# Performance work log

Hardware: AMD Instinct MI355X
Metric: run time of the kernel (lower is better)

## Reference

```python
import jax, jax.numpy as jnp
import numpy as np

B, S, D, H = 2, 2048, 1024, 16
DK = D // H

def setup_inputs() -> dict:
    key = jax.random.key(0)
    ks = jax.random.split(key, 9)
    sc = 1.0 / np.sqrt(D)
    return {
        "query": jax.random.normal(ks[0], (B, S, D), jnp.float32),
        "key_": jax.random.normal(ks[1], (B, S, D), jnp.float32),
        "value": jax.random.normal(ks[2], (B, S, D), jnp.float32),
        "Wq": jax.random.normal(ks[3], (D, D), jnp.float32) * sc,
        "bq": jnp.zeros((D,), jnp.float32),
        "Wk": jax.random.normal(ks[4], (D, D), jnp.float32) * sc,
        "bk": jnp.zeros((D,), jnp.float32),
        "Wv": jax.random.normal(ks[5], (D, D), jnp.float32) * sc,
        "bv": jnp.zeros((D,), jnp.float32),
    }

def reference(query, key_, value, Wq, bq, Wk, bk, Wv, bv):
    # QKV projections -> [B, H, S, DK]
    def heads(x, W, b):
        return (x @ W + b).reshape(B, S, H, DK).transpose(0, 2, 1, 3)
    q = heads(query, Wq, bq)
    k = heads(key_, Wk, bk)
    v = heads(value, Wv, bv)
    scores = jnp.einsum('bhsd,bhtd->bhst', q, k) / jnp.sqrt(jnp.float32(DK))
    attn = jax.nn.softmax(scores, axis=-1)  # dropout = identity (eval)
    ctx = jnp.einsum('bhst,bhtd->bhsd', attn, v)
    return ctx.transpose(0, 2, 1, 3).reshape(B, S, D)
```

## Files before the change

### kernel.cpp

```cpp
#include <hip/hip_runtime.h>
#include <hip/hip_bf16.h>

typedef __bf16 bf16x4 __attribute__((ext_vector_type(4)));
typedef __bf16 bf16x8 __attribute__((ext_vector_type(8)));
typedef float  f32x4  __attribute__((ext_vector_type(4)));
typedef float  f32x16 __attribute__((ext_vector_type(16)));

constexpr int B = 2, S = 2048, D = 1024, H = 16, DK = 64;
constexpr int M = B * S;
constexpr int BH = B * H;

__device__ inline float fexp2(float x) {
#if __has_builtin(__builtin_amdgcn_exp2f)
  return __builtin_amdgcn_exp2f(x);
#else
  return exp2f(x);
#endif
}
__device__ inline float frcp(float x) {
#if __has_builtin(__builtin_amdgcn_rcpf)
  return __builtin_amdgcn_rcpf(x);
#else
  return 1.0f / x;
#endif
}
__device__ inline unsigned pk2(float lo, float hi) {
  union { __bf16 h[2]; unsigned u; } x;
  x.h[0] = (__bf16)lo; x.h[1] = (__bf16)hi;
  return x.u;
}

__global__ __launch_bounds__(256) void wtrans3(const float* __restrict__ w0,
                                               const float* __restrict__ w1,
                                               const float* __restrict__ w2,
                                               __bf16* __restrict__ t0,
                                               __bf16* __restrict__ t1,
                                               __bf16* __restrict__ t2) {
  int z = blockIdx.z;
  const float* W = z == 0 ? w0 : z == 1 ? w1 : w2;
  __bf16* WT = z == 0 ? t0 : z == 1 ? t1 : t2;
  __shared__ float t[32][33];
  int tx = threadIdx.x & 31, ty0 = threadIdx.x >> 5;
  int n0 = blockIdx.x * 32, k0 = blockIdx.y * 32;
#pragma unroll
  for (int i = 0; i < 4; ++i)
    t[ty0 + i * 8][tx] = W[(size_t)(k0 + ty0 + i * 8) * D + n0 + tx];
  __syncthreads();
#pragma unroll
  for (int i = 0; i < 4; ++i)
    WT[(size_t)(n0 + ty0 + i * 8) * D + k0 + tx] = (__bf16)t[tx][ty0 + i * 8];
}

constexpr int TM = 128, TN = 128, BK = 64;

__global__ __launch_bounds__(256, 3) void proj3(
    const float* __restrict__ X0, const float* __restrict__ X1,
    const float* __restrict__ X2, const __bf16* __restrict__ W0,
    const __bf16* __restrict__ W1, const __bf16* __restrict__ W2,
    const float* __restrict__ b0, const float* __restrict__ b1,
    const float* __restrict__ b2, __bf16* __restrict__ Qo,
    __bf16* __restrict__ Ko, __bf16* __restrict__ Vo) {
  __shared__ __align__(16) __bf16 As[TM * BK];
  __shared__ __align__(16) __bf16 Bs[2][TN * BK];
  int z = blockIdx.z;
  const float* A   = z == 0 ? X0 : z == 1 ? X1 : X2;
  const __bf16* BT = z == 0 ? W0 : z == 1 ? W1 : W2;
  const float* bias = z == 0 ? b0 : z == 1 ? b1 : b2;
  __bf16* out = z == 0 ? Qo : z == 1 ? Ko : Vo;
  int mode = (z == 2) ? 1 : 0;
  float osc = (z == 0) ? 0.18033688011112042f : 1.0f;

  int t = threadIdx.x;
  int fid = blockIdx.x;
  int xcd = fid & 7, slot = fid >> 3;
  int m0 = (xcd * 4 + (slot >> 3)) * TM;
  int n0 = (slot & 7) * TN;
  int w = t >> 6, lane = t & 63, c = lane & 15, g = lane >> 4;
  int wr = w >> 1, wc = w & 1;

  f32x4 acc[4][4];
#pragma unroll
  for (int i = 0; i < 4; ++i)
#pragma unroll
    for (int j = 0; j < 4; ++j) acc[i][j] = f32x4{0.f, 0.f, 0.f, 0.f};

  int srcoff = (((t & 7) ^ ((t >> 3) & 7)) << 4);
  int srow = t >> 3;
  const float* aptr[4];
  const __bf16* bptr[4];
#pragma unroll
  for (int i = 0; i < 4; ++i) {
    aptr[i] = A + (size_t)(m0 + i * 32 + srow) * D + (srcoff >> 1);
    bptr[i] = BT + (size_t)(n0 + i * 32 + srow) * D + (srcoff >> 1);
  }

  float4 pa[4][2];
#pragma unroll
  for (int i = 0; i < 4; ++i) {
    pa[i][0] = *(const float4*)(aptr[i]);
    pa[i][1] = *(const float4*)(aptr[i] + 4);
  }
#pragma unroll
  for (int i = 0; i < 4; ++i)
    __builtin_amdgcn_global_load_lds(
        (const __attribute__((address_space(1))) unsigned int*)(bptr[i]),
        (__attribute__((address_space(3))) unsigned int*)((char*)&Bs[0][0] + i * 4096 + t * 16), 16, 0, 0);

  int rswz = ((c & 7) << 4);

  int buf = 0;
  for (int kk = 0; kk < D; kk += BK, buf ^= 1) {
    if (kk + BK < D) {
#pragma unroll
      for (int i = 0; i < 4; ++i)
        __builtin_amdgcn_global_load_lds(
            (const __attribute__((address_space(1))) unsigned int*)(bptr[i] + kk + BK),
            (__attribute__((address_space(3))) unsigned int*)((char*)&Bs[buf ^ 1][0] + i * 4096 + t * 16), 16, 0, 0);
    }
#pragma unroll
    for (int i = 0; i < 4; ++i) {
      bf16x8 v;
      v[0] = (__bf16)pa[i][0].x; v[1] = (__bf16)pa[i][0].y;
      v[2] = (__bf16)pa[i][0].z; v[3] = (__bf16)pa[i][0].w;
      v[4] = (__bf16)pa[i][1].x; v[5] = (__bf16)pa[i][1].y;
      v[6] = (__bf16)pa[i][1].z; v[7] = (__bf16)pa[i][1].w;
      *(bf16x8*)((char*)As + i * 4096 + t * 16) = v;
    }
    if (kk + BK < D)
      asm volatile("s_waitcnt vmcnt(4) lgkmcnt(0)" ::: "memory");
    else
      asm volatile("s_waitcnt vmcnt(0) lgkmcnt(0)" ::: "memory");
    __builtin_amdgcn_s_barrier();
    __builtin_amdgcn_sched_barrier(0);

    if (kk + BK < D) {
#pragma unroll
      for (int i = 0; i < 4; ++i) {
        pa[i][0] = *(const float4*)(aptr[i] + kk + BK);
        pa[i][1] = *(const float4*)(aptr[i] + kk + BK + 4);
      }
    }

#pragma unroll
    for (int ks = 0; ks < 2; ++ks) {
      int cb = (ks * 64 + g * 16) ^ rswz;
      bf16x8 af[4], bf[4];
#pragma unroll
      for (int i = 0; i < 4; ++i)
        af[i] = *(const bf16x8*)((char*)As + (wr * 64 + i * 16 + c) * 128 + cb);
#pragma unroll
      for (int j = 0; j < 4; ++j)
        bf[j] = *(const bf16x8*)((char*)&Bs[buf][0] + (wc * 64 + j * 16 + c) * 128 + cb);
#pragma unroll
      for (int i = 0; i < 4; ++i)
#pragma unroll
        for (int j = 0; j < 4; ++j)
          acc[i][j] = __builtin_amdgcn_mfma_f32_16x16x32_bf16(af[i], bf[j], acc[i][j], 0, 0, 0);
    }

    asm volatile("s_waitcnt lgkmcnt(0)" ::: "memory");
    __builtin_amdgcn_s_barrier();
    __builtin_amdgcn_sched_barrier(0);
  }

#pragma unroll
  for (int i = 0; i < 4; ++i)
#pragma unroll
    for (int j = 0; j < 4; ++j) {
      int n = n0 + wc * 64 + j * 16 + c;
      float bv = bias[n];
      int h = n >> 6, dk = n & 63;
#pragma unroll
      for (int q = 0; q < 4; ++q) {
        int mrow = m0 + wr * 64 + i * 16 + g * 4 + q;
        int b = mrow >> 11, s = mrow & (S - 1);
        float val = (acc[i][j][q] + bv) * osc;
        size_t idx;
        if (mode == 0) idx = ((size_t)(b * H + h) * S + s) * DK + dk;
        else           idx = ((size_t)(b * H + h) * DK + dk) * S + s;
        out[idx] = (__bf16)val;
      }
    }
}

constexpr int NSTEP = S / 64;

__global__ __launch_bounds__(256) void attn(const __bf16* __restrict__ Q,
                                            const __bf16* __restrict__ K,
                                            const __bf16* __restrict__ VT,
                                            float* __restrict__ out) {
  __shared__ __align__(16) __bf16 Ks[2][4096];
  __shared__ __align__(16) __bf16 Vs[2][4096];

  int t = threadIdx.x, w = t >> 6, lane = t & 63;
  int l31 = lane & 31, hi = lane >> 5;

  int fid = blockIdx.x;
  int xcd = fid & 7, slot = fid >> 3;
  int bh = xcd * 4 + (slot >> 4);
  int q0 = (slot & 15) * 128 + w * 32;

  const __bf16* Qb = Q + (size_t)bh * S * DK;
  const char* Kg = (const char*)(K + (size_t)bh * S * DK);
  const char* Vg = (const char*)(VT + (size_t)bh * DK * S);

  bf16x8 qf[4];
  {
    const __bf16* qp = Qb + (size_t)(q0 + l31) * DK + hi * 8;
#pragma unroll
    for (int s2 = 0; s2 < 4; ++s2) qf[s2] = *(const bf16x8*)(qp + s2 * 16);
  }

  f32x16 ZERO;
#pragma unroll
  for (int r = 0; r < 16; ++r) ZERO[r] = 0.f;

  f32x16 acc0, acc1;
#pragma unroll
  for (int r = 0; r < 16; ++r) { acc0[r] = 0.f; acc1[r] = 0.f; }
  float lrun = 0.f;

  int krow = ((l31 >> 2) & 1) * 8 + ((l31 >> 3) & 1) * 16 + ((l31 >> 4) & 1) * 4 + (l31 & 3);
  int kswz = (((krow & 7) ^ ((krow >> 3) & 3)) << 4);
  int vswz = (((l31 & 7) ^ ((l31 >> 3) & 3)) << 4);

  auto stage = [&](int bufi, int kstep) {
#pragma unroll
    for (int i = 0; i < 2; ++i) {
      int L = i * 4096 + t * 16;
      int row = L >> 7;
      int sz = (((row & 7) ^ ((row >> 3) & 3)) << 4);
      __builtin_amdgcn_global_load_lds(
          (const __attribute__((address_space(1))) unsigned int*)(Kg + (size_t)kstep * 8192 + (L ^ sz)),
          (__attribute__((address_space(3))) unsigned int*)((char*)&Ks[bufi][0] + L), 16, 0, 0);
      __builtin_amdgcn_global_load_lds(
          (const __attribute__((address_space(1))) unsigned int*)(Vg + (size_t)row * (S * 2) + kstep * 128 + ((L & 127) ^ sz)),
          (__attribute__((address_space(3))) unsigned int*)((char*)&Vs[bufi][0] + L), 16, 0, 0);
    }
  };

  auto loadFrag = [&](const char* kb, const char* vb, int sub, bf16x8* Kf, bf16x8* Vf) {
    const char* kr = kb + ((sub * 32 + krow) << 7);
#pragma unroll
    for (int s2 = 0; s2 < 4; ++s2)
      Kf[s2] = *(const bf16x8*)(kr + ((s2 * 32 + hi * 16) ^ kswz));
#pragma unroll
    for (int ks = 0; ks < 2; ++ks)
#pragma unroll
      for (int db = 0; db < 2; ++db)
        Vf[ks * 2 + db] = *(const bf16x8*)(vb + ((db * 32 + l31) << 7) +
                                           ((sub * 64 + ks * 32 + hi * 16) ^ vswz));
  };

  auto computeQK = [&](bf16x8* Kf) -> f32x16 {
    __builtin_amdgcn_s_setprio(1);
    f32x16 st = __builtin_amdgcn_mfma_f32_32x32x16_bf16(Kf[0], qf[0], ZERO, 0, 0, 0);
    st = __builtin_amdgcn_mfma_f32_32x32x16_bf16(Kf[1], qf[1], st, 0, 0, 0);
    st = __builtin_amdgcn_mfma_f32_32x32x16_bf16(Kf[2], qf[2], st, 0, 0, 0);
    st = __builtin_amdgcn_mfma_f32_32x32x16_bf16(Kf[3], qf[3], st, 0, 0, 0);
    __builtin_amdgcn_s_setprio(0);
    return st;
  };

  auto computeSMPV = [&](const f32x16& st, bf16x8* Vf) {
    float p[16];
#pragma unroll
    for (int r = 0; r < 16; ++r) p[r] = fexp2(st[r]);
    {
      float t0 = (p[0] + p[1]) + (p[2] + p[3]);
      float t1 = (p[4] + p[5]) + (p[6] + p[7]);
      float t2 = (p[8] + p[9]) + (p[10] + p[11]);
      float t3 = (p[12] + p[13]) + (p[14] + p[15]);
      lrun += (t0 + t1) + (t2 + t3);
    }
    union Pk { unsigned u[4]; bf16x8 v; } P0, P1;
    P0.u[0] = pk2(p[0], p[1]);   P0.u[1] = pk2(p[2], p[3]);
    P0.u[2] = pk2(p[8], p[9]);   P0.u[3] = pk2(p[10], p[11]);
    P1.u[0] = pk2(p[4], p[5]);   P1.u[1] = pk2(p[6], p[7]);
    P1.u[2] = pk2(p[12], p[13]); P1.u[3] = pk2(p[14], p[15]);

    __builtin_amdgcn_s_setprio(1);
    acc0 = __builtin_amdgcn_mfma_f32_32x32x16_bf16(P0.v, Vf[0], acc0, 0, 0, 0);
    acc1 = __builtin_amdgcn_mfma_f32_32x32x16_bf16(P0.v, Vf[1], acc1, 0, 0, 0);
    acc0 = __builtin_amdgcn_mfma_f32_32x32x16_bf16(P1.v, Vf[2], acc0, 0, 0, 0);
    acc1 = __builtin_amdgcn_mfma_f32_32x32x16_bf16(P1.v, Vf[3], acc1, 0, 0, 0);
    __builtin_amdgcn_s_setprio(0);
  };

  stage(0, 0);
  __syncthreads();

  bf16x8 KfA[4], VfA[4], KfB[4], VfB[4];
  for (int tt = 0; tt < NSTEP; ++tt) {
    int cur = tt & 1;
    if (tt + 1 < NSTEP) stage(cur ^ 1, tt + 1);
    const char* kb = (const char*)&Ks[cur][0];
    const char* vb = (const char*)&Vs[cur][0];

    loadFrag(kb, vb, 0, KfA, VfA);
    loadFrag(kb, vb, 1, KfB, VfB);
    f32x16 stA = computeQK(KfA);
    f32x16 stB = computeQK(KfB);
    computeSMPV(stA, VfA);
    computeSMPV(stB, VfB);

    __syncthreads();
  }

  lrun += __shfl_xor(lrun, 32);
  int b = bh >> 4, h = bh & 15;
#pragma unroll
  for (int r = 0; r < 16; ++r) {
    int rowq = (r & 3) + 8 * (r >> 2) + 4 * hi;
    float li = __shfl(lrun, rowq);
    float ri = frcp(li);
    size_t base = (size_t)(b * S + q0 + rowq) * D + h * 64 + l31;
    out[base] = acc0[r] * ri;
    out[base + 32] = acc1[r] * ri;
  }
}

extern "C" void kernel_launch(void* const* d_in, const int* in_sizes, int n_in,
                              void* d_out, int out_size, void* d_ws, size_t ws_size,
                              hipStream_t stream) {
  (void)in_sizes; (void)n_in; (void)out_size; (void)ws_size;
  const float* xq = (const float*)d_in[0];
  const float* xk = (const float*)d_in[1];
  const float* xv = (const float*)d_in[2];
  const float* Wq = (const float*)d_in[3];
  const float* bq = (const float*)d_in[4];
  const float* Wk = (const float*)d_in[5];
  const float* bk = (const float*)d_in[6];
  const float* Wv = (const float*)d_in[7];
  const float* bv = (const float*)d_in[8];

  char* ws = (char*)d_ws;
  const size_t MB = 1u << 20;
  __bf16* WT[3] = {(__bf16*)(ws + 24 * MB), (__bf16*)(ws + 26 * MB), (__bf16*)(ws + 28 * MB)};
  __bf16* Qb = (__bf16*)(ws + 30 * MB);
  __bf16* Kb = (__bf16*)(ws + 38 * MB);
  __bf16* Vt = (__bf16*)(ws + 46 * MB);

  wtrans3<<<dim3(D / 32, D / 32, 3), 256, 0, stream>>>(Wq, Wk, Wv, WT[0], WT[1], WT[2]);
  proj3<<<dim3(256, 1, 3), 256, 0, stream>>>(xq, xk, xv,
                                             WT[0], WT[1], WT[2],
                                             bq, bk, bv, Qb, Kb, Vt);
  attn<<<dim3(512), 256, 0, stream>>>(Qb, Kb, Vt, (float*)d_out);
}
```

Before: 100.2 us.

## Split key range across two wave groups per attention block and merge in LDS

The attention kernel now launches 512 threads per block. Two groups of four waves each process half of the key/value sequence for the same 128 queries, with separate double-buffered LDS regions. At the end, the second group writes its partial accumulators and row sums to shared memory, and the first group adds them and normalizes. This halves the serial KV loop per wave and raises waves in flight to hide latency. The costs are more LDS per block, block-wide barriers across eight waves, and an extra reduction step.

```diff
diff --git a/kernel.cpp b/kernel.cpp
--- a/kernel.cpp
+++ b/kernel.cpp
@@ -183,26 +183,31 @@
     }
 }
 
-constexpr int NSTEP = S / 64;
-
-__global__ __launch_bounds__(256) void attn(const __bf16* __restrict__ Q,
+constexpr int HKV = S / 2;
+constexpr int NSTEP = HKV / 64;
+
+__global__ __launch_bounds__(512) void attn(const __bf16* __restrict__ Q,
                                             const __bf16* __restrict__ K,
                                             const __bf16* __restrict__ VT,
                                             float* __restrict__ out) {
-  __shared__ __align__(16) __bf16 Ks[2][4096];
-  __shared__ __align__(16) __bf16 Vs[2][4096];
+  __shared__ __align__(16) char smem[65536];
 
   int t = threadIdx.x, w = t >> 6, lane = t & 63;
+  int half = w >> 2, wl = w & 3;
   int l31 = lane & 31, hi = lane >> 5;
+  int th = t & 255;
 
   int fid = blockIdx.x;
   int xcd = fid & 7, slot = fid >> 3;
   int bh = xcd * 4 + (slot >> 4);
-  int q0 = (slot & 15) * 128 + w * 32;
+  int q0 = (slot & 15) * 128 + wl * 32;
 
   const __bf16* Qb = Q + (size_t)bh * S * DK;
-  const char* Kg = (const char*)(K + (size_t)bh * S * DK);
-  const char* Vg = (const char*)(VT + (size_t)bh * DK * S);
+  const char* Kg = (const char*)(K + (size_t)bh * S * DK) + (size_t)half * HKV * DK * 2;
+  const char* Vg = (const char*)(VT + (size_t)bh * DK * S) + (size_t)half * HKV * 2;
+
+  char* kbase = smem + half * 32768;
+  char* vbase = smem + half * 32768 + 16384;
 
   bf16x8 qf[4];
   {
@@ -227,15 +232,15 @@
   auto stage = [&](int bufi, int kstep) {
 #pragma unroll
     for (int i = 0; i < 2; ++i) {
-      int L = i * 4096 + t * 16;
+      int L = i * 4096 + th * 16;
       int row = L >> 7;
       int sz = (((row & 7) ^ ((row >> 3) & 3)) << 4);
       __builtin_amdgcn_global_load_lds(
           (const __attribute__((address_space(1))) unsigned int*)(Kg + (size_t)kstep * 8192 + (L ^ sz)),
-          (__attribute__((address_space(3))) unsigned int*)((char*)&Ks[bufi][0] + L), 16, 0, 0);
+          (__attribute__((address_space(3))) unsigned int*)(kbase + bufi * 8192 + L), 16, 0, 0);
       __builtin_amdgcn_global_load_lds(
           (const __attribute__((address_space(1))) unsigned int*)(Vg + (size_t)row * (S * 2) + kstep * 128 + ((L & 127) ^ sz)),
-          (__attribute__((address_space(3))) unsigned int*)((char*)&Vs[bufi][0] + L), 16, 0, 0);
+          (__attribute__((address_space(3))) unsigned int*)(vbase + bufi * 8192 + L), 16, 0, 0);
     }
   };
 
@@ -294,8 +299,8 @@
   for (int tt = 0; tt < NSTEP; ++tt) {
     int cur = tt & 1;
     if (tt + 1 < NSTEP) stage(cur ^ 1, tt + 1);
-    const char* kb = (const char*)&Ks[cur][0];
-    const char* vb = (const char*)&Vs[cur][0];
+    const char* kb = kbase + cur * 8192;
+    const char* vb = vbase + cur * 8192;
 
     loadFrag(kb, vb, 0, KfA, VfA);
     loadFrag(kb, vb, 1, KfB, VfB);
@@ -308,15 +313,32 @@
   }
 
   lrun += __shfl_xor(lrun, 32);
-  int b = bh >> 4, h = bh & 15;
-#pragma unroll
-  for (int r = 0; r < 16; ++r) {
-    int rowq = (r & 3) + 8 * (r >> 2) + 4 * hi;
-    float li = __shfl(lrun, rowq);
-    float ri = frcp(li);
-    size_t base = (size_t)(b * S + q0 + rowq) * D + h * 64 + l31;
-    out[base] = acc0[r] * ri;
-    out[base + 32] = acc1[r] * ri;
+  __syncthreads();
+
+  float* xch = (float*)smem;
+  int xi = (wl * 64 + lane) * 33;
+  if (half == 1) {
+#pragma unroll
+    for (int r = 0; r < 16; ++r) {
+      xch[xi + r] = acc0[r];
+      xch[xi + 16 + r] = acc1[r];
+    }
+    xch[xi + 32] = lrun;
+  }
+  __syncthreads();
+
+  if (half == 0) {
+    float lt = lrun + xch[xi + 32];
+    int b = bh >> 4, h = bh & 15;
+#pragma unroll
+    for (int r = 0; r < 16; ++r) {
+      int rowq = (r & 3) + 8 * (r >> 2) + 4 * hi;
+      float li = __shfl(lt, rowq);
+      float ri = frcp(li);
+      size_t base = (size_t)(b * S + q0 + rowq) * D + h * 64 + l31;
+      out[base] = (acc0[r] + xch[xi + r]) * ri;
+      out[base + 32] = (acc1[r] + xch[xi + 16 + r]) * ri;
+    }
   }
 }
 
@@ -345,5 +367,5 @@
   proj3<<<dim3(256, 1, 3), 256, 0, stream>>>(xq, xk, xv,
                                              WT[0], WT[1], WT[2],
                                              bq, bk, bv, Qb, Kb, Vt);
-  attn<<<dim3(512), 256, 0, stream>>>(Qb, Kb, Vt, (float*)d_out);
-}
+  attn<<<dim3(512), 512, 0, stream>>>(Qb, Kb, Vt, (float*)d_out);
+}
```

Result: faster. 93.45 us (median of 2 runs) (-6.8%).
